# Kernel optimization log

Measured on AMD Instinct MI355X. Metric: run time of the kernel, lower is better.

## Reference

```python
import jax, jax.numpy as jnp
import numpy as np

B, T, E, H = 32, 512, 512, 1024


def setup_inputs() -> dict:
    key = jax.random.key(0)
    k1, k2, k3 = jax.random.split(key, 3)
    s_ih = 1.0 / np.sqrt(E)
    s_hh = 1.0 / np.sqrt(H)
    return {
        "x": jax.random.normal(k1, (B, T, E), dtype=jnp.float32),
        "h0": jnp.zeros((B, H), dtype=jnp.float32),
        "w_ih": jax.random.normal(k2, (3 * H, E), dtype=jnp.float32) * s_ih,
        "w_hh": jax.random.normal(k3, (3 * H, H), dtype=jnp.float32) * s_hh,
    }


def reference(x, h0, w_ih, w_hh):
    # GRU recurrence (no biases, matching the module's parameters).
    # Precompute input projections for all timesteps in one big GEMM.
    xg = jnp.einsum("bte,ge->btg", x, w_ih)  # [B, T, 3H]
    xg = jnp.swapaxes(xg, 0, 1)               # [T, B, 3H] for scan

    def step(h, xg_t):
        hg = h @ w_hh.T                        # [B, 3H]
        ir, iz, i_n = jnp.split(xg_t, 3, axis=-1)
        hr, hz, h_n = jnp.split(hg, 3, axis=-1)
        r = jax.nn.sigmoid(ir + hr)            # reset gate
        z = jax.nn.sigmoid(iz + hz)            # update gate
        n = jnp.tanh(i_n + r * h_n)            # candidate state
        h_new = (1.0 - z) * n + z * h
        return h_new, h_new

    _, ys = jax.lax.scan(step, h0, xg)         # ys: [T, B, H]
    return jnp.swapaxes(ys, 0, 1)              # [B, T, H]
```

## Files before the change

kernel.cpp:

```cpp
#include <hip/hip_runtime.h>
#include <cmath>


namespace {
constexpr int BATCH  = 32;
constexpr int TSTEPS = 512;
constexpr int EDIM   = 512;
constexpr int HDIM   = 1024;
constexpr int GDIM   = 3 * HDIM;
constexpr int SLOT   = HDIM * BATCH;

constexpr size_t XG_BYTES    = (size_t)TSTEPS * GDIM * BATCH * 4;
constexpr size_t FLAGS_BYTES = 4096;
constexpr size_t SLOT_BYTES  = (size_t)SLOT * 4;
constexpr size_t HBUF_BYTES  = SLOT_BYTES;
}

__global__ __launch_bounds__(256)
void xg_gemm_f32(const float* __restrict__ x, const float* __restrict__ w_ih,
                 float* __restrict__ xgt)
{
    __shared__ float a_s[16 * 132];
    __shared__ float b_s[16 * 132];

    const int tid = threadIdx.x;
    const int n0 = blockIdx.x * 128;
    const int m0 = blockIdx.y * 128;
    const int tx = tid & 15;
    const int ty = tid >> 4;

    float acc[8][8];
    #pragma unroll
    for (int i = 0; i < 8; ++i)
        #pragma unroll
        for (int j = 0; j < 8; ++j) acc[i][j] = 0.f;

    const int r_ld = tid >> 2;
    const int kq4  = (tid & 3) * 4;

    for (int kc = 0; kc < EDIM; kc += 16) {
        __syncthreads();
        #pragma unroll
        for (int half = 0; half < 2; ++half) {
            const int r = r_ld + half * 64;
            const int m = m0 + r;
            const int bb = m & 31;
            const int tt = m >> 5;
            float4 av = *(const float4*)&x[((size_t)bb * TSTEPS + tt) * EDIM + kc + kq4];
            a_s[(kq4 + 0) * 132 + r] = av.x;
            a_s[(kq4 + 1) * 132 + r] = av.y;
            a_s[(kq4 + 2) * 132 + r] = av.z;
            a_s[(kq4 + 3) * 132 + r] = av.w;
            const int n = n0 + r;
            float4 bv = *(const float4*)&w_ih[(size_t)n * EDIM + kc + kq4];
            b_s[(kq4 + 0) * 132 + r] = bv.x;
            b_s[(kq4 + 1) * 132 + r] = bv.y;
            b_s[(kq4 + 2) * 132 + r] = bv.z;
            b_s[(kq4 + 3) * 132 + r] = bv.w;
        }
        __syncthreads();
        #pragma unroll
        for (int k = 0; k < 16; ++k) {
            float a_r[8], b_r[8];
            *(float4*)&a_r[0] = *(const float4*)&a_s[k * 132 + ty * 8];
            *(float4*)&a_r[4] = *(const float4*)&a_s[k * 132 + ty * 8 + 4];
            *(float4*)&b_r[0] = *(const float4*)&b_s[k * 132 + tx * 8];
            *(float4*)&b_r[4] = *(const float4*)&b_s[k * 132 + tx * 8 + 4];
            #pragma unroll
            for (int i = 0; i < 8; ++i)
                #pragma unroll
                for (int j = 0; j < 8; ++j)
                    acc[i][j] = fmaf(a_r[i], b_r[j], acc[i][j]);
        }
    }

    const int t  = (m0 >> 5) + (ty >> 2);
    const int b0 = (ty & 3) * 8;
    #pragma unroll
    for (int j = 0; j < 8; ++j) {
        const int g    = n0 + tx * 8 + j;
        const int gate = g >> 10;
        const int jj   = g & 1023;
        float* p = &xgt[(((size_t)t * 3 + gate) * 1024 + jj) * 32 + b0];
        *(float4*)p       = make_float4(acc[0][j], acc[1][j], acc[2][j], acc[3][j]);
        *(float4*)(p + 4) = make_float4(acc[4][j], acc[5][j], acc[6][j], acc[7][j]);
    }
}

__global__ __launch_bounds__(1024, 4)
void gru_ring(const float* __restrict__ h0, const float* __restrict__ w_hh,
              const float* __restrict__ xgt, float* __restrict__ out,
              float* __restrict__ ring, unsigned* __restrict__ flags,
              int nslot)
{
    __shared__ float w_s[12 * 1032];
    __shared__ float red_s[16 * 8 * 83];

    const int tid = threadIdx.x;
    const int bid = blockIdx.x;
    const int j0  = bid * 4;

    for (int i = tid; i < 12 * 256; i += 1024) {
        const int row  = i >> 8;
        const int c4   = (i & 255) * 4;
        const int gate = row >> 2;
        const int jl   = row & 3;
        *(float4*)&w_s[row * 1032 + c4] =
            *(const float4*)&w_hh[((size_t)gate * HDIM + j0 + jl) * HDIM + c4];
    }

    const int tjl = tid >> 5;
    const int tb  = tid & 31;

    float hp = 0.f, hnew = 0.f;
    if (tid < 128) {
        hp = h0[(size_t)tb * HDIM + j0 + tjl];
        __hip_atomic_store(&ring[(j0 + tjl) * 32 + tb], hp,
                           __ATOMIC_RELAXED, __HIP_MEMORY_SCOPE_AGENT);
    }

    __syncthreads();
    if (tid < 64) __builtin_amdgcn_fence(__ATOMIC_ACQUIRE, "agent");
    __syncthreads();

    if (tid == 0)
        __hip_atomic_store(&flags[bid], 1u,
                           __ATOMIC_RELAXED, __HIP_MEMORY_SCOPE_AGENT);

    float xr = 0.f, xz = 0.f, xn = 0.f;
    if (tid < 128) {
        const size_t base = (size_t)(j0 + tjl) * 32 + tb;
        xr = xgt[base];
        xz = xgt[base + 32768];
        xn = xgt[base + 65536];
    }

    if (tid < 64) {
        for (;;) {
            unsigned a0 = __hip_atomic_load(&flags[tid],       __ATOMIC_RELAXED, __HIP_MEMORY_SCOPE_AGENT);
            unsigned a1 = __hip_atomic_load(&flags[tid + 64],  __ATOMIC_RELAXED, __HIP_MEMORY_SCOPE_AGENT);
            unsigned a2 = __hip_atomic_load(&flags[tid + 128], __ATOMIC_RELAXED, __HIP_MEMORY_SCOPE_AGENT);
            unsigned a3 = __hip_atomic_load(&flags[tid + 192], __ATOMIC_RELAXED, __HIP_MEMORY_SCOPE_AGENT);
            unsigned m01 = a0 < a1 ? a0 : a1;
            unsigned m23 = a2 < a3 ? a2 : a3;
            unsigned mn  = m01 < m23 ? m01 : m23;
            if (__all(mn >= 1u)) break;
            __builtin_amdgcn_s_sleep(1);
        }
    }
    __syncthreads();

    const int bgrp  = tid & 7;
    const int kseg  = tid >> 3;
    const int b0    = bgrp * 4;
    const int kbase = kseg * 8;
    const int wvi   = tid >> 6;
    const int h3  = (tid >> 3) & 1;
    const int h4b = (tid >> 4) & 1;
    const int h5  = (tid >> 5) & 1;
    const int rbase = 6 * h3 + 3 * h4b;
    const int bb2   = 2 * h5;

    int slot = 0;
    int next_fence = nslot;

    for (int t = 0; t < TSTEPS; ++t) {
        const float* sp = ring + (size_t)slot * SLOT;
        const int slot_nx = (slot + 1 == nslot) ? 0 : slot + 1;

        float4 hv[8];
        #pragma unroll
        for (int i = 0; i < 8; ++i)
            hv[i] = *(const float4*)&sp[(kbase + i) * 32 + b0];

        float acc[12][4];
        #pragma unroll
        for (int r = 0; r < 12; ++r)
            #pragma unroll
            for (int b = 0; b < 4; ++b) acc[r][b] = 0.f;

        #pragma unroll
        for (int q = 0; q < 2; ++q)
            #pragma unroll
            for (int r = 0; r < 12; ++r) {
                const float4 w4 = *(const float4*)&w_s[r * 1032 + kbase + q * 4];
                const float wq[4] = {w4.x, w4.y, w4.z, w4.w};
                #pragma unroll
                for (int i = 0; i < 4; ++i) {
                    const float4 h4i = hv[q * 4 + i];
                    acc[r][0] = fmaf(wq[i], h4i.x, acc[r][0]);
                    acc[r][1] = fmaf(wq[i], h4i.y, acc[r][1]);
                    acc[r][2] = fmaf(wq[i], h4i.z, acc[r][2]);
                    acc[r][3] = fmaf(wq[i], h4i.w, acc[r][3]);
                }
            }

        float a6[6][4];
        #pragma unroll
        for (int m = 0; m < 6; ++m)
            #pragma unroll
            for (int b = 0; b < 4; ++b) {
                const float send = h3 ? acc[m][b] : acc[6 + m][b];
                const float recv = __shfl_xor(send, 8, 64);
                a6[m][b] = (h3 ? acc[6 + m][b] : acc[m][b]) + recv;
            }
        float a3[3][4];
        #pragma unroll
        for (int m = 0; m < 3; ++m)
            #pragma unroll
            for (int b = 0; b < 4; ++b) {
                const float send = h4b ? a6[m][b] : a6[3 + m][b];
                const float recv = __shfl_xor(send, 16, 64);
                a3[m][b] = (h4b ? a6[3 + m][b] : a6[m][b]) + recv;
            }
        float a2[3][2];
        #pragma unroll
        for (int m = 0; m < 3; ++m)
            #pragma unroll
            for (int b = 0; b < 2; ++b) {
                const float send = h5 ? a3[m][b] : a3[m][2 + b];
                const float recv = __shfl_xor(send, 32, 64);
                a2[m][b] = (h5 ? a3[m][2 + b] : a3[m][b]) + recv;
            }
        {
            float* dst = &red_s[(wvi * 8 + bgrp) * 83];
            #pragma unroll
            for (int m = 0; m < 3; ++m) {
                dst[(rbase + m) * 4 + bb2 + 0] = a2[m][0];
                dst[(rbase + m) * 4 + bb2 + 1] = a2[m][1];
            }
        }
        __syncthreads();

        if (tid < 128) {
            const int bg = tb >> 2, bs = tb & 3;
            float s0 = 0.f, s1 = 0.f, s2 = 0.f;
            #pragma unroll
            for (int w = 0; w < 16; ++w) {
                const float* rs = &red_s[(w * 8 + bg) * 83 + bs];
                s0 += rs[(0 * 4 + tjl) * 4];
                s1 += rs[(1 * 4 + tjl) * 4];
                s2 += rs[(2 * 4 + tjl) * 4];
            }
            const float rg   = 1.f / (1.f + expf(-(xr + s0)));
            const float zg   = 1.f / (1.f + expf(-(xz + s1)));
            const float ng   = tanhf(xn + rg * s2);
            hnew = (1.f - zg) * ng + zg * hp;
            hp = hnew;
            if (t + 1 < TSTEPS)
                __hip_atomic_store(&ring[(size_t)slot_nx * SLOT + (j0 + tjl) * 32 + tb],
                                   hnew, __ATOMIC_RELAXED, __HIP_MEMORY_SCOPE_AGENT);
        }

        __syncthreads();

        if (t + 1 < TSTEPS) {
            if (tid == 0)
                __hip_atomic_store(&flags[bid], (unsigned)(t + 2),
                                   __ATOMIC_RELAXED, __HIP_MEMORY_SCOPE_AGENT);

            if (tid < 128) {
                out[((size_t)tb * TSTEPS + t) * HDIM + j0 + tjl] = hnew;
                const size_t b2 = ((size_t)(t + 1) * 3072 + (j0 + tjl)) * 32 + tb;
                xr = xgt[b2];
                xz = xgt[b2 + 32768];
                xn = xgt[b2 + 65536];
            }

            if (tid < 64) {
                const unsigned tgt = (unsigned)(t + 2);
                for (;;) {
                    unsigned a0 = __hip_atomic_load(&flags[tid],       __ATOMIC_RELAXED, __HIP_MEMORY_SCOPE_AGENT);
                    unsigned a1 = __hip_atomic_load(&flags[tid + 64],  __ATOMIC_RELAXED, __HIP_MEMORY_SCOPE_AGENT);
                    unsigned a2 = __hip_atomic_load(&flags[tid + 128], __ATOMIC_RELAXED, __HIP_MEMORY_SCOPE_AGENT);
                    unsigned a3 = __hip_atomic_load(&flags[tid + 192], __ATOMIC_RELAXED, __HIP_MEMORY_SCOPE_AGENT);
                    unsigned m01 = a0 < a1 ? a0 : a1;
                    unsigned m23 = a2 < a3 ? a2 : a3;
                    unsigned mn  = m01 < m23 ? m01 : m23;
                    if (__all(mn >= tgt)) break;
                    __builtin_amdgcn_s_sleep(1);
                }
            }
            __syncthreads();

            if (t + 1 == next_fence) {
                if (tid < 64) __builtin_amdgcn_fence(__ATOMIC_ACQUIRE, "agent");
                __syncthreads();
                next_fence += nslot;
            }
        } else {
            if (tid < 128)
                out[((size_t)tb * TSTEPS + t) * HDIM + j0 + tjl] = hnew;
        }

        slot = slot_nx;
    }
}

__global__ __launch_bounds__(1024, 4)
void gru_recurrence(const float* __restrict__ h0, const float* __restrict__ w_hh,
                    const float* __restrict__ xgt, float* __restrict__ out,
                    float* __restrict__ hbufA, float* __restrict__ hbufB,
                    unsigned* __restrict__ flags)
{
    __shared__ float w_s[12 * 1032];
    __shared__ float red_s[16 * 8 * 83];

    const int tid = threadIdx.x;
    const int bid = blockIdx.x;
    const int j0  = bid * 4;

    for (int i = tid; i < 12 * 256; i += 1024) {
        const int row  = i >> 8;
        const int c4   = (i & 255) * 4;
        const int gate = row >> 2;
        const int jl   = row & 3;
        *(float4*)&w_s[row * 1032 + c4] =
            *(const float4*)&w_hh[((size_t)gate * HDIM + j0 + jl) * HDIM + c4];
    }

    const int tjl = tid >> 5;
    const int tb  = tid & 31;

    float hp = 0.f, hnew = 0.f;
    if (tid < 128) {
        hp = h0[(size_t)tb * HDIM + j0 + tjl];
        __hip_atomic_store(&hbufA[(j0 + tjl) * 32 + tb], hp,
                           __ATOMIC_RELAXED, __HIP_MEMORY_SCOPE_AGENT);
    }

    __syncthreads();
    if (tid == 0)
        __hip_atomic_store(&flags[tid + bid * 8], 1u,
                           __ATOMIC_RELAXED, __HIP_MEMORY_SCOPE_AGENT);

    float xr = 0.f, xz = 0.f, xn = 0.f;
    if (tid < 128) {
        const size_t base = (size_t)(j0 + tjl) * 32 + tb;
        xr = xgt[base];
        xz = xgt[base + 32768];
        xn = xgt[base + 65536];
    }
    if (tid < 256) {
        const unsigned* fp = &flags[tid * 8];
        while (__hip_atomic_load(fp, __ATOMIC_RELAXED, __HIP_MEMORY_SCOPE_AGENT) < 1u)
            __builtin_amdgcn_s_sleep(2);
    }
    __syncthreads();

    const int bgrp  = tid & 7;
    const int kseg  = tid >> 3;
    const int b0    = bgrp * 4;
    const int kbase = kseg * 8;
    const int wvi   = tid >> 6;
    const int h3  = (tid >> 3) & 1;
    const int h4b = (tid >> 4) & 1;
    const int h5  = (tid >> 5) & 1;
    const int rbase = 6 * h3 + 3 * h4b;
    const int bb2   = 2 * h5;

    for (int t = 0; t < TSTEPS; ++t) {
        const float* hcur = (t & 1) ? hbufB : hbufA;
        float* hnxt       = (t & 1) ? hbufA : hbufB;

        float4 hv[8];
        #pragma unroll
        for (int i = 0; i < 8; ++i) {
            const float* p = &hcur[(kbase + i) * 32 + b0];
            unsigned long long lo = __hip_atomic_load(
                (const unsigned long long*)p, __ATOMIC_RELAXED, __HIP_MEMORY_SCOPE_AGENT);
            unsigned long long hi = __hip_atomic_load(
                (const unsigned long long*)(p + 2), __ATOMIC_RELAXED, __HIP_MEMORY_SCOPE_AGENT);
            hv[i].x = __uint_as_float((unsigned)lo);
            hv[i].y = __uint_as_float((unsigned)(lo >> 32));
            hv[i].z = __uint_as_float((unsigned)hi);
            hv[i].w = __uint_as_float((unsigned)(hi >> 32));
        }

        float acc[12][4];
        #pragma unroll
        for (int r = 0; r < 12; ++r)
            #pragma unroll
            for (int b = 0; b < 4; ++b) acc[r][b] = 0.f;

        #pragma unroll
        for (int q = 0; q < 2; ++q)
            #pragma unroll
            for (int r = 0; r < 12; ++r) {
                const float4 w4 = *(const float4*)&w_s[r * 1032 + kbase + q * 4];
                const float wq[4] = {w4.x, w4.y, w4.z, w4.w};
                #pragma unroll
                for (int i = 0; i < 4; ++i) {
                    const float4 h4i = hv[q * 4 + i];
                    acc[r][0] = fmaf(wq[i], h4i.x, acc[r][0]);
                    acc[r][1] = fmaf(wq[i], h4i.y, acc[r][1]);
                    acc[r][2] = fmaf(wq[i], h4i.z, acc[r][2]);
                    acc[r][3] = fmaf(wq[i], h4i.w, acc[r][3]);
                }
            }

        float a6[6][4];
        #pragma unroll
        for (int m = 0; m < 6; ++m)
            #pragma unroll
            for (int b = 0; b < 4; ++b) {
                const float send = h3 ? acc[m][b] : acc[6 + m][b];
                const float recv = __shfl_xor(send, 8, 64);
                a6[m][b] = (h3 ? acc[6 + m][b] : acc[m][b]) + recv;
            }
        float a3[3][4];
        #pragma unroll
        for (int m = 0; m < 3; ++m)
            #pragma unroll
            for (int b = 0; b < 4; ++b) {
                const float send = h4b ? a6[m][b] : a6[3 + m][b];
                const float recv = __shfl_xor(send, 16, 64);
                a3[m][b] = (h4b ? a6[3 + m][b] : a6[m][b]) + recv;
            }
        float a2[3][2];
        #pragma unroll
        for (int m = 0; m < 3; ++m)
            #pragma unroll
            for (int b = 0; b < 2; ++b) {
                const float send = h5 ? a3[m][b] : a3[m][2 + b];
                const float recv = __shfl_xor(send, 32, 64);
                a2[m][b] = (h5 ? a3[m][2 + b] : a3[m][b]) + recv;
            }
        {
            float* dst = &red_s[(wvi * 8 + bgrp) * 83];
            #pragma unroll
            for (int m = 0; m < 3; ++m) {
                dst[(rbase + m) * 4 + bb2 + 0] = a2[m][0];
                dst[(rbase + m) * 4 + bb2 + 1] = a2[m][1];
            }
        }
        __syncthreads();

        if (tid < 128) {
            const int bg = tb >> 2, bs = tb & 3;
            float s0 = 0.f, s1 = 0.f, s2 = 0.f;
            #pragma unroll
            for (int w = 0; w < 16; ++w) {
                const float* rs = &red_s[(w * 8 + bg) * 83 + bs];
                s0 += rs[(0 * 4 + tjl) * 4];
                s1 += rs[(1 * 4 + tjl) * 4];
                s2 += rs[(2 * 4 + tjl) * 4];
            }
            const float rg   = 1.f / (1.f + expf(-(xr + s0)));
            const float zg   = 1.f / (1.f + expf(-(xz + s1)));
            const float ng   = tanhf(xn + rg * s2);
            hnew = (1.f - zg) * ng + zg * hp;
            hp = hnew;
            __hip_atomic_store(&hnxt[(j0 + tjl) * 32 + tb], hnew,
                               __ATOMIC_RELAXED, __HIP_MEMORY_SCOPE_AGENT);
        }

        __syncthreads();
        if (tid == 0)
            __hip_atomic_store(&flags[bid * 8], (unsigned)(t + 2),
                               __ATOMIC_RELAXED, __HIP_MEMORY_SCOPE_AGENT);

        if (tid < 128) {
            out[((size_t)tb * TSTEPS + t) * HDIM + j0 + tjl] = hnew;
            if (t + 1 < TSTEPS) {
                const size_t b2 = ((size_t)(t + 1) * 3072 + (j0 + tjl)) * 32 + tb;
                xr = xgt[b2];
                xz = xgt[b2 + 32768];
                xn = xgt[b2 + 65536];
            }
        }

        if (t + 1 < TSTEPS) {
            if (tid < 256) {
                const unsigned* fp = &flags[tid * 8];
                while (__hip_atomic_load(fp, __ATOMIC_RELAXED, __HIP_MEMORY_SCOPE_AGENT)
                       < (unsigned)(t + 2))
                    __builtin_amdgcn_s_sleep(2);
            }
            __syncthreads();
        }
    }
}

extern "C" void kernel_launch(void* const* d_in, const int* in_sizes, int n_in,
                              void* d_out, int out_size, void* d_ws, size_t ws_size,
                              hipStream_t stream)
{
    const float* x    = (const float*)d_in[0];
    const float* h0   = (const float*)d_in[1];
    const float* w_ih = (const float*)d_in[2];
    const float* w_hh = (const float*)d_in[3];
    float* out = (float*)d_out;

    char* ws = (char*)d_ws;
    float* xgt = (float*)ws;

    dim3 g1(GDIM / 128, (BATCH * TSTEPS) / 128);
    xg_gemm_f32<<<g1, 256, 0, stream>>>(x, w_ih, xgt);

    size_t avail = (ws_size > XG_BYTES + FLAGS_BYTES)
                       ? (ws_size - XG_BYTES - FLAGS_BYTES) : 0;
    int nslot = (int)(avail / SLOT_BYTES);
    if (nslot > TSTEPS) nslot = TSTEPS;

    if (nslot >= 64) {
        unsigned* flags = (unsigned*)(ws + XG_BYTES);
        float* ring     = (float*)(ws + XG_BYTES + FLAGS_BYTES);
        hipMemsetAsync(flags, 0, FLAGS_BYTES, stream);
        gru_ring<<<256, 1024, 0, stream>>>(h0, w_hh, xgt, out, ring, flags, nslot);
    } else {
        float* hbufA    = (float*)(ws + XG_BYTES);
        float* hbufB    = (float*)(ws + XG_BYTES + HBUF_BYTES);
        unsigned* flags = (unsigned*)(ws + XG_BYTES + 2 * HBUF_BYTES);
        hipMemsetAsync(flags, 0, 256 * 8 * sizeof(unsigned), stream);
        gru_recurrence<<<256, 1024, 0, stream>>>(h0, w_hh, xgt, out, hbufA, hbufB, flags);
    }
}
```

Before: 3.439 ms.

## Replace block-wide flag barrier with per-wave dependency polling in GRU ring kernel

Each wave now spins only on the 16 producer-block flags whose hidden-state rows it actually reads, at the start of the step. This replaces the wave-0 poll over all 256 flags plus two block barriers. The reduction scratch buffer is double-buffered by timestep parity, which drops the trailing __syncthreads per step. The flag is published right after an s_waitcnt on the ring store. The aim is to cut global-barrier latency on the sequential critical path, but tid 0 only waits on its own wave's stores, so wave 1's ring writes may not be visible when the flag is raised.

New measurement: 5.319 ms. 54.7% more time.

```diff
diff --git a/kernel.cpp b/kernel.cpp
--- a/kernel.cpp
+++ b/kernel.cpp
@@ -94,7 +94,7 @@
               int nslot)
 {
     __shared__ float w_s[12 * 1032];
-    __shared__ float red_s[16 * 8 * 83];
+    __shared__ float red_s[2][16 * 8 * 83];
 
     const int tid = threadIdx.x;
     const int bid = blockIdx.x;
@@ -122,7 +122,6 @@
     __syncthreads();
     if (tid < 64) __builtin_amdgcn_fence(__ATOMIC_ACQUIRE, "agent");
     __syncthreads();
-
     if (tid == 0)
         __hip_atomic_store(&flags[bid], 1u,
                            __ATOMIC_RELAXED, __HIP_MEMORY_SCOPE_AGENT);
@@ -135,26 +134,14 @@
         xn = xgt[base + 65536];
     }
 
-    if (tid < 64) {
-        for (;;) {
-            unsigned a0 = __hip_atomic_load(&flags[tid],       __ATOMIC_RELAXED, __HIP_MEMORY_SCOPE_AGENT);
-            unsigned a1 = __hip_atomic_load(&flags[tid + 64],  __ATOMIC_RELAXED, __HIP_MEMORY_SCOPE_AGENT);
-            unsigned a2 = __hip_atomic_load(&flags[tid + 128], __ATOMIC_RELAXED, __HIP_MEMORY_SCOPE_AGENT);
-            unsigned a3 = __hip_atomic_load(&flags[tid + 192], __ATOMIC_RELAXED, __HIP_MEMORY_SCOPE_AGENT);
-            unsigned m01 = a0 < a1 ? a0 : a1;
-            unsigned m23 = a2 < a3 ? a2 : a3;
-            unsigned mn  = m01 < m23 ? m01 : m23;
-            if (__all(mn >= 1u)) break;
-            __builtin_amdgcn_s_sleep(1);
-        }
-    }
-    __syncthreads();
+    const int wv   = tid >> 6;
+    const int lane = tid & 63;
+    const unsigned* const myflag = &flags[16 * wv + (lane & 15)];
 
     const int bgrp  = tid & 7;
     const int kseg  = tid >> 3;
     const int b0    = bgrp * 4;
     const int kbase = kseg * 8;
-    const int wvi   = tid >> 6;
     const int h3  = (tid >> 3) & 1;
     const int h4b = (tid >> 4) & 1;
     const int h5  = (tid >> 5) & 1;
@@ -165,8 +152,23 @@
     int next_fence = nslot;
 
     for (int t = 0; t < TSTEPS; ++t) {
+        const int slot_nx = (slot + 1 == nslot) ? 0 : slot + 1;
+
+        {
+            const unsigned tgt = (unsigned)(t + 1);
+            for (;;) {
+                unsigned f = __hip_atomic_load(myflag, __ATOMIC_RELAXED,
+                                               __HIP_MEMORY_SCOPE_AGENT);
+                if (__all(f >= tgt)) break;
+                __builtin_amdgcn_s_sleep(1);
+            }
+        }
+        if (t == next_fence) {
+            __builtin_amdgcn_fence(__ATOMIC_ACQUIRE, "agent");
+            next_fence += nslot;
+        }
+
         const float* sp = ring + (size_t)slot * SLOT;
-        const int slot_nx = (slot + 1 == nslot) ? 0 : slot + 1;
 
         float4 hv[8];
         #pragma unroll
@@ -223,21 +225,23 @@
                 a2[m][b] = (h5 ? a3[m][2 + b] : a3[m][b]) + recv;
             }
         {
-            float* dst = &red_s[(wvi * 8 + bgrp) * 83];
+            float* dst = &red_s[t & 1][(wv * 8 + bgrp) * 83];
             #pragma unroll
             for (int m = 0; m < 3; ++m) {
                 dst[(rbase + m) * 4 + bb2 + 0] = a2[m][0];
                 dst[(rbase + m) * 4 + bb2 + 1] = a2[m][1];
             }
         }
+
         __syncthreads();
 
         if (tid < 128) {
             const int bg = tb >> 2, bs = tb & 3;
+            const float* rbuf = red_s[t & 1];
             float s0 = 0.f, s1 = 0.f, s2 = 0.f;
             #pragma unroll
             for (int w = 0; w < 16; ++w) {
-                const float* rs = &red_s[(w * 8 + bg) * 83 + bs];
+                const float* rs = &rbuf[(w * 8 + bg) * 83 + bs];
                 s0 += rs[(0 * 4 + tjl) * 4];
                 s1 += rs[(1 * 4 + tjl) * 4];
                 s2 += rs[(2 * 4 + tjl) * 4];
@@ -247,50 +251,22 @@
             const float ng   = tanhf(xn + rg * s2);
             hnew = (1.f - zg) * ng + zg * hp;
             hp = hnew;
-            if (t + 1 < TSTEPS)
+
+            if (t + 1 < TSTEPS) {
                 __hip_atomic_store(&ring[(size_t)slot_nx * SLOT + (j0 + tjl) * 32 + tb],
                                    hnew, __ATOMIC_RELAXED, __HIP_MEMORY_SCOPE_AGENT);
-        }
-
-        __syncthreads();
-
-        if (t + 1 < TSTEPS) {
-            if (tid == 0)
-                __hip_atomic_store(&flags[bid], (unsigned)(t + 2),
-                                   __ATOMIC_RELAXED, __HIP_MEMORY_SCOPE_AGENT);
-
-            if (tid < 128) {
+                asm volatile("s_waitcnt vmcnt(0)" ::: "memory");
+                if (tid == 0)
+                    __hip_atomic_store(&flags[bid], (unsigned)(t + 2),
+                                       __ATOMIC_RELAXED, __HIP_MEMORY_SCOPE_AGENT);
                 out[((size_t)tb * TSTEPS + t) * HDIM + j0 + tjl] = hnew;
                 const size_t b2 = ((size_t)(t + 1) * 3072 + (j0 + tjl)) * 32 + tb;
                 xr = xgt[b2];
                 xz = xgt[b2 + 32768];
                 xn = xgt[b2 + 65536];
-            }
-
-            if (tid < 64) {
-                const unsigned tgt = (unsigned)(t + 2);
-                for (;;) {
-                    unsigned a0 = __hip_atomic_load(&flags[tid],       __ATOMIC_RELAXED, __HIP_MEMORY_SCOPE_AGENT);
-                    unsigned a1 = __hip_atomic_load(&flags[tid + 64],  __ATOMIC_RELAXED, __HIP_MEMORY_SCOPE_AGENT);
-                    unsigned a2 = __hip_atomic_load(&flags[tid + 128], __ATOMIC_RELAXED, __HIP_MEMORY_SCOPE_AGENT);
-                    unsigned a3 = __hip_atomic_load(&flags[tid + 192], __ATOMIC_RELAXED, __HIP_MEMORY_SCOPE_AGENT);
-                    unsigned m01 = a0 < a1 ? a0 : a1;
-                    unsigned m23 = a2 < a3 ? a2 : a3;
-                    unsigned mn  = m01 < m23 ? m01 : m23;
-                    if (__all(mn >= tgt)) break;
-                    __builtin_amdgcn_s_sleep(1);
-                }
-            }
-            __syncthreads();
-
-            if (t + 1 == next_fence) {
-                if (tid < 64) __builtin_amdgcn_fence(__ATOMIC_ACQUIRE, "agent");
-                __syncthreads();
-                next_fence += nslot;
-            }
-        } else {
-            if (tid < 128)
+            } else {
                 out[((size_t)tb * TSTEPS + t) * HDIM + j0 + tjl] = hnew;
+            }
         }
 
         slot = slot_nx;
@@ -331,7 +307,7 @@
 
     __syncthreads();
     if (tid == 0)
-        __hip_atomic_store(&flags[tid + bid * 8], 1u,
+        __hip_atomic_store(&flags[bid * 8], 1u,
                            __ATOMIC_RELAXED, __HIP_MEMORY_SCOPE_AGENT);
 
     float xr = 0.f, xz = 0.f, xn = 0.f;
```
